# Kernel optimization log

Measured on AMD Instinct MI355X. Metric: run time of the kernel, lower is better.

Reference implementation:

```python
import jax, jax.numpy as jnp
import numpy as np

B, T, D, H = 128, 512, 64, 512  # batch, seq_len, feature dim, hidden dim
S_MIN, S_FRAC = 0.5, 0.5        # aug_args for generate_samp_mask


def setup_inputs() -> dict:
    key = jax.random.key(0)
    ks = jax.random.split(key, 8)
    x = jax.random.normal(ks[0], (B, T, D), jnp.float32)
    # monotonically increasing irregular timestamps
    tp = jnp.cumsum(jax.random.uniform(ks[1], (B, T), jnp.float32, 1e-3, 0.1), axis=1)
    # Deterministic replay of generate_samp_mask: mask[i]=1 -> teacher forcing
    rng = np.random.default_rng(0)
    extrap_ind = int(rng.integers(int(T * S_MIN), T))
    samp_inds = np.sort(rng.choice(np.arange(extrap_ind), int(S_FRAC * extrap_ind), replace=False))
    mask = np.zeros(T, dtype=np.int32)
    mask[samp_inds] = 1
    samp_mask = jnp.asarray(mask)
    s = 1.0 / np.sqrt(H)  # torch GRUCell/Linear default uniform init scale
    W_ih = jax.random.uniform(ks[2], (3 * H, D + 1), jnp.float32, -s, s)
    W_hh = jax.random.uniform(ks[3], (3 * H, H), jnp.float32, -s, s)
    b_ih = jax.random.uniform(ks[4], (3 * H,), jnp.float32, -s, s)
    b_hh = jax.random.uniform(ks[5], (3 * H,), jnp.float32, -s, s)
    W_out = jax.random.uniform(ks[6], (H, D), jnp.float32, -s, s)
    b_out = jax.random.uniform(ks[7], (D,), jnp.float32, -s, s)
    return {"x": x, "tp": tp, "samp_mask": samp_mask, "W_ih": W_ih, "W_hh": W_hh,
            "b_ih": b_ih, "b_hh": b_hh, "W_out": W_out, "b_out": b_out}


def _gru_cell(inp, h, W_ih, W_hh, b_ih, b_hh):
    gi = inp @ W_ih.T + b_ih          # (B, 3H)
    gh = h @ W_hh.T + b_hh            # (B, 3H)
    i_r, i_z, i_n = jnp.split(gi, 3, axis=-1)
    h_r, h_z, h_n = jnp.split(gh, 3, axis=-1)
    r = jax.nn.sigmoid(i_r + h_r)
    z = jax.nn.sigmoid(i_z + h_z)
    n = jnp.tanh(i_n + r * h_n)
    return (1.0 - z) * n + z * h


def reference(x, tp, samp_mask, W_ih, W_hh, b_ih, b_hh, W_out, b_out):
    # delta_t: append time deltas as an extra channel
    offset = jnp.concatenate([jnp.zeros((tp.shape[0], 1), tp.dtype), tp[:, :-1]], axis=1)
    delta = (tp - offset)[..., None]            # (B, T, 1)
    xin = jnp.concatenate([x, delta], axis=-1)  # (B, T, D+1)

    def step(h, inputs):
        x_t, m = inputs                          # (B, D+1), scalar bool
        prev_out = h @ W_out + b_out             # (B, D)
        ar_in = jnp.concatenate([prev_out, x_t[:, -2:-1]], axis=-1)  # (B, D+1)
        inp = jnp.where(m, x_t, ar_in)
        h_new = _gru_cell(inp, h, W_ih, W_hh, b_ih, b_hh)
        return h_new, h_new

    h0 = jnp.zeros((x.shape[0], H), x.dtype)
    _, h_arr = jax.lax.scan(step, h0, (jnp.swapaxes(xin, 0, 1), samp_mask.astype(bool)))
    h_arr = jnp.swapaxes(h_arr, 0, 1)            # (B, T, H)
    out = h_arr @ W_out + b_out                  # (B, T, D)
    # select_by_length with lens == T for every sample -> flat (B*T, D)
    return out.reshape(-1, out.shape[-1])
```

## Files before the change

kernel.cpp:

```cpp
#include <hip/hip_runtime.h>
#include <math.h>

#define TB 512

typedef __attribute__((ext_vector_type(8))) short bf16x8;
typedef __attribute__((ext_vector_type(4))) float f32x4;
typedef unsigned long long u64;

#define BW_B   0
#define AH_B   98304
#define PRE_F  32768
#define XPRE_F 33824
#define ORED_F 34616
#define WOC_F  35160
#define WIH_F  35672
#define SB_F   37256
#define XLAST_F 37352
#define MSK_F  37384
#define LDS_FLOATS 37896
#define LDS_BYTES (LDS_FLOATS * 4)

#define STEP_BYTES 262144
#define GRP_BYTES  65536
#define HIST_NEEDED (4096ull + 513ull * STEP_BYTES)
#define PLANE_STRIDE 262144
#define FB_NEEDED (4096ull + 2ull * PLANE_STRIDE)

__device__ __forceinline__ unsigned rne16(float f) {
  unsigned u = __float_as_uint(f);
  return (u + 0x7FFFu + ((u >> 16) & 1u)) >> 16;
}
__device__ __forceinline__ float bfhilo(unsigned hh, unsigned hl) {
  return __uint_as_float(hh << 16) + __uint_as_float(hl << 16);
}

__global__ __launch_bounds__(TB) void gru_persistent(
    const float* __restrict__ x, const float* __restrict__ tp, const int* __restrict__ mask,
    const float* __restrict__ W_ih, const float* __restrict__ W_hh,
    const float* __restrict__ b_ih, const float* __restrict__ b_hh,
    const float* __restrict__ W_out, const float* __restrict__ b_out,
    char* __restrict__ data, unsigned* __restrict__ ctr,
    float* __restrict__ out, int hmode)
{
  extern __shared__ char smem[];
  float* LP = (float*)smem;
  int* MSK = (int*)&LP[MSK_F];
  const int tid = threadIdx.x;
  const int wg  = blockIdx.x;
  const int s   = wg & 63;
  const int g   = wg >> 6;
  const int bg0 = g * 32;
  const int j0  = 8 * s;
  const int lane = tid & 63;
  const int wv   = tid >> 6;

  unsigned short* planes = (unsigned short*)data;

  MSK[tid] = mask[tid];
  if (tid < 65) {
    for (int p = 0; p < 24; ++p) {
      int row = (p < 8) ? (j0 + p) : (p < 16) ? (512 + j0 + (p - 8)) : (1024 + j0 + (p - 16));
      LP[WIH_F + p * 66 + tid] = W_ih[(size_t)row * 65 + tid];
    }
  }
  LP[WOC_F + tid] = W_out[(size_t)tid * 64 + s];
  if (tid < 16) {
    int row = (tid < 8) ? (j0 + tid) : (512 + j0 + (tid - 8));
    const float* wi = W_ih + (size_t)row * 65;
    float bt = b_ih[row] + b_hh[row];
    float bp = 0.f;
    for (int d = 0; d < 64; ++d) bp = fmaf(wi[d], b_out[d], bp);
    LP[SB_F + tid]      = bt;
    LP[SB_F + 16 + tid] = bt + bp;
    LP[SB_F + 32 + tid] = wi[64];
  } else if (tid < 24) {
    int jj = tid - 16;
    int row = 1024 + j0 + jj;
    const float* wi = W_ih + (size_t)row * 65;
    float bp = 0.f;
    for (int d = 0; d < 64; ++d) bp = fmaf(wi[d], b_out[d], bp);
    LP[SB_F + 48 + jj] = b_hh[row];
    LP[SB_F + 56 + jj] = b_ih[row];
    LP[SB_F + 64 + jj] = b_ih[row] + bp;
    LP[SB_F + 72 + jj] = wi[64];
  }
  if (tid == 0) LP[SB_F + 80] = b_out[s];

  if (tid < 32) {
    if (hmode) {
      const int half = tid >> 4, ln = (tid & 15) | ((s & 3) << 4), ks = s >> 2;
      char* dst = data + (size_t)g * GRP_BYTES;
      u64* c0 = (u64*)(dst + (size_t)(((0 * 16 + ks) * 2 + half) * 64 + ln) * 16);
      u64* c1 = (u64*)(dst + (size_t)(((1 * 16 + ks) * 2 + half) * 64 + ln) * 16);
      __hip_atomic_store(c0,     0ull, __ATOMIC_RELAXED, __HIP_MEMORY_SCOPE_AGENT);
      __hip_atomic_store(c0 + 1, 0ull, __ATOMIC_RELAXED, __HIP_MEMORY_SCOPE_AGENT);
      __hip_atomic_store(c1,     0ull, __ATOMIC_RELAXED, __HIP_MEMORY_SCOPE_AGENT);
      __hip_atomic_store(c1 + 1, 0ull, __ATOMIC_RELAXED, __HIP_MEMORY_SCOPE_AGENT);
    } else {
      u64* hh0 = (u64*)(planes + (size_t)(bg0 + tid) * 512 + j0);
      u64* hl0 = (u64*)(planes + 65536 + (size_t)(bg0 + tid) * 512 + j0);
      __hip_atomic_store(hh0,     0ull, __ATOMIC_RELAXED, __HIP_MEMORY_SCOPE_AGENT);
      __hip_atomic_store(hh0 + 1, 0ull, __ATOMIC_RELAXED, __HIP_MEMORY_SCOPE_AGENT);
      __hip_atomic_store(hl0,     0ull, __ATOMIC_RELAXED, __HIP_MEMORY_SCOPE_AGENT);
      __hip_atomic_store(hl0 + 1, 0ull, __ATOMIC_RELAXED, __HIP_MEMORY_SCOPE_AGENT);
    }
  }
  __syncthreads();

  {
    const int k = tid;
    const float* wo = W_out + (size_t)k * 64;
    unsigned short* bw16 = (unsigned short*)(smem + BW_B);
    for (int rr = 0; rr < 48; ++rr) {
      int c, col; float w;
      if (rr < 16) {
        c = 1; col = rr;
        int row = (rr < 8) ? (j0 + rr) : (512 + j0 + rr - 8);
        w = W_hh[(size_t)row * 512 + k];
      } else if (rr < 24) {
        c = 0; col = rr - 16;
        w = W_hh[(size_t)(1024 + j0 + rr - 16) * 512 + k];
      } else {
        int p, whrow;
        if (rr < 32) { c = 0; col = rr - 24 + 8; p = 16 + (rr - 24); whrow = -1; }
        else if (rr < 40) { c = 2; col = rr - 32; p = rr - 32; whrow = j0 + rr - 32; }
        else { c = 2; col = rr - 40 + 8; p = 8 + (rr - 40); whrow = 512 + j0 + rr - 40; }
        const float* wr = &LP[WIH_F + p * 66];
        float a = 0.f;
#pragma unroll 8
        for (int d = 0; d < 64; ++d) a = fmaf(wr[d], wo[d], a);
        w = a + (whrow >= 0 ? W_hh[(size_t)whrow * 512 + k] : 0.f);
      }
      unsigned wh = rne16(w);
      float resid = w - __uint_as_float(wh << 16);
      unsigned wl = rne16(resid);
      int base = c * 32768 + (k >> 5) * 1024 + (col | (((k >> 3) & 3) << 4)) * 16 + (k & 7) * 2;
      bw16[base >> 1] = (unsigned short)wh;
      bw16[(base + 16384) >> 1] = (unsigned short)wl;
    }
  }
  __syncthreads();

  auto stage_x = [&](int tt) {
    if (tt >= 512) return;
    if (MSK[tt] != 0) {
      for (int task = tid; task < 768; task += TB) {
        const int xr = task >> 5, b = task & 31;
        const float* wrow = &LP[WIH_F + xr * 66];
        size_t ti = (size_t)(bg0 + b) * 512 + tt;
        float del = tp[ti] - (tt > 0 ? tp[ti - 1] : 0.f);
        float xa = wrow[64] * del;
        const float4* x4 = (const float4*)(x + ti * 64);
#pragma unroll
        for (int d4 = 0; d4 < 16; ++d4) {
          float4 xv = x4[d4];
          xa = fmaf(wrow[d4 * 4 + 0], xv.x, xa);
          xa = fmaf(wrow[d4 * 4 + 1], xv.y, xa);
          xa = fmaf(wrow[d4 * 4 + 2], xv.z, xa);
          xa = fmaf(wrow[d4 * 4 + 3], xv.w, xa);
        }
        LP[XPRE_F + xr * 33 + b] = xa;
      }
    } else if (tid < 32) {
      LP[XLAST_F + tid] = x[((size_t)(bg0 + tid) * 512 + tt) * 64 + 63];
    }
  };

  stage_x(0);

  unsigned target = 64;
  unsigned* myctr = &ctr[g * 64];

  asm volatile("s_waitcnt vmcnt(0)" ::: "memory");
  __syncthreads();
  if (tid == 0) {
    __hip_atomic_fetch_add(myctr, 1u, __ATOMIC_RELAXED, __HIP_MEMORY_SCOPE_AGENT);
    int cnt = 0;
    while (__hip_atomic_load(myctr, __ATOMIC_RELAXED, __HIP_MEMORY_SCOPE_AGENT) < target) {
      __builtin_amdgcn_s_sleep(2);
      if (++cnt > 16384) break;
    }
  }
  __syncthreads();
  target += 64;

  const unsigned short* ah16 = (const unsigned short*)(smem + AH_B);

  for (int t = 0; t <= 512; ++t) {
    const bool last = (t == 512);
    const bool teacher = (!last) && (MSK[t] != 0);
    const int csel = teacher ? 1 : 2;

    uint4 h0v[4], h1v[4];
    if (hmode) {
      const char* src = data + (size_t)t * STEP_BYTES + (size_t)g * GRP_BYTES;
#pragma unroll
      for (int i = 0; i < 4; ++i) {
        int c = i * 512 + tid;
        int sg = c >> 6, ln = c & 63;
        h0v[i] = *(const uint4*)(src + (size_t)((sg * 2 + 0) * 64 + ln) * 16);
        h1v[i] = *(const uint4*)(src + (size_t)((sg * 2 + 1) * 64 + ln) * 16);
      }
    } else {
      const int cur = t & 1;
      const unsigned short* HHc = planes + (size_t)cur * (PLANE_STRIDE / 2);
      const unsigned short* HLc = HHc + 65536;
#pragma unroll
      for (int i = 0; i < 4; ++i) {
        int c = i * 512 + tid;
        int sg = c >> 6, ln = c & 63;
        int term = sg >> 4, ks = sg & 15;
        const unsigned short* pl = term ? HLc : HHc;
        const unsigned short* src0 = pl + ((size_t)(bg0 + (ln & 15)) * 512 + ks * 32 + ((ln >> 4) & 3) * 8);
        const u64* p0 = (const u64*)src0;
        const u64* p1 = (const u64*)(src0 + 16 * 512);
        u64 a0 = __hip_atomic_load(p0,     __ATOMIC_RELAXED, __HIP_MEMORY_SCOPE_AGENT);
        u64 a1 = __hip_atomic_load(p0 + 1, __ATOMIC_RELAXED, __HIP_MEMORY_SCOPE_AGENT);
        u64 b0 = __hip_atomic_load(p1,     __ATOMIC_RELAXED, __HIP_MEMORY_SCOPE_AGENT);
        u64 b1 = __hip_atomic_load(p1 + 1, __ATOMIC_RELAXED, __HIP_MEMORY_SCOPE_AGENT);
        h0v[i] = uint4{(unsigned)a0, (unsigned)(a0 >> 32), (unsigned)a1, (unsigned)(a1 >> 32)};
        h1v[i] = uint4{(unsigned)b0, (unsigned)(b0 >> 32), (unsigned)b1, (unsigned)(b1 >> 32)};
      }
    }
#pragma unroll
    for (int i = 0; i < 4; ++i) {
      int c = i * 512 + tid;
      *(uint4*)(smem + AH_B + (size_t)c * 16) = h0v[i];
    }
    __syncthreads();

    float hp = 0.f;
    for (int half = 0; half < 2; ++half) {
      const int rtoff = half * 16;

      if (!last && wv < 2) {
        const int cslot = (wv == 0) ? 0 : csel;
        const char* bb = smem + BW_B + cslot * 32768;
        const char* ab = smem + AH_B;
        f32x4 acc0 = {0.f, 0.f, 0.f, 0.f};
        f32x4 acc1 = {0.f, 0.f, 0.f, 0.f};
        f32x4 acc2 = {0.f, 0.f, 0.f, 0.f};
        f32x4 acc3 = {0.f, 0.f, 0.f, 0.f};
#pragma unroll
        for (int ks4 = 0; ks4 < 4; ++ks4) {
#pragma unroll
          for (int q4 = 0; q4 < 4; ++q4) {
            int ks = ks4 * 4 + q4;
            bf16x8 ahh = *(const bf16x8*)(ab + ks * 1024 + lane * 16);
            bf16x8 ahl = *(const bf16x8*)(ab + (16 + ks) * 1024 + lane * 16);
            bf16x8 bhh = *(const bf16x8*)(bb + ks * 1024 + lane * 16);
            bf16x8 bhl = *(const bf16x8*)(bb + (16 + ks) * 1024 + lane * 16);
            f32x4& acc = (q4 == 0) ? acc0 : (q4 == 1) ? acc1 : (q4 == 2) ? acc2 : acc3;
            acc = __builtin_amdgcn_mfma_f32_16x16x32_bf16(ahh, bhh, acc, 0, 0, 0);
            acc = __builtin_amdgcn_mfma_f32_16x16x32_bf16(ahh, bhl, acc, 0, 0, 0);
            acc = __builtin_amdgcn_mfma_f32_16x16x32_bf16(ahl, bhh, acc, 0, 0, 0);
          }
        }
        f32x4 accA = acc0 + acc1;
        f32x4 accB = acc2 + acc3;
        f32x4 acc = accA + accB;
        const int prow = ((wv == 0) ? 16 : 0) + (lane & 15);
        const int pcol = rtoff + ((lane >> 4) << 2);
#pragma unroll
        for (int q = 0; q < 4; ++q) LP[PRE_F + prow * 33 + pcol + q] = acc[q];
      }

      if (tid >= 128 && tid < 384) {
        const int tA = tid - 128;
        const int bl = tA & 15, ks = tA >> 4;
        const int b = rtoff + bl;
        const float* woc = &LP[WOC_F];
        float oa = 0.f;
#pragma unroll
        for (int c = 0; c < 4; ++c) {
          const uint4 wh = *(const uint4*)(smem + AH_B + ks * 1024 + (bl | (c << 4)) * 16);
          const uint4 wl = *(const uint4*)(smem + AH_B + (16 + ks) * 1024 + (bl | (c << 4)) * 16);
          int k0 = ks * 32 + c * 8;
          oa = fmaf(bfhilo(wh.x & 0xFFFFu, wl.x & 0xFFFFu), woc[k0 + 0], oa);
          oa = fmaf(bfhilo(wh.x >> 16, wl.x >> 16), woc[k0 + 1], oa);
          oa = fmaf(bfhilo(wh.y & 0xFFFFu, wl.y & 0xFFFFu), woc[k0 + 2], oa);
          oa = fmaf(bfhilo(wh.y >> 16, wl.y >> 16), woc[k0 + 3], oa);
          oa = fmaf(bfhilo(wh.z & 0xFFFFu, wl.z & 0xFFFFu), woc[k0 + 4], oa);
          oa = fmaf(bfhilo(wh.z >> 16, wl.z >> 16), woc[k0 + 5], oa);
          oa = fmaf(bfhilo(wh.w & 0xFFFFu, wl.w & 0xFFFFu), woc[k0 + 6], oa);
          oa = fmaf(bfhilo(wh.w >> 16, wl.w >> 16), woc[k0 + 7], oa);
        }
        LP[ORED_F + b * 17 + ks] = oa;
      }

      if (tid < 256 && (((tid & 31) >> 4) == half)) {
        const int b = tid & 31, jj = tid >> 5;
        const int k = j0 + jj;
        const int ks = k >> 5, e = k & 7;
        const int ln = (b & 15) | (((k >> 3) & 3) << 4);
        unsigned hh = ah16[(ks * 1024 + ln * 16 + e * 2) >> 1];
        unsigned hl = ah16[((16 + ks) * 1024 + ln * 16 + e * 2) >> 1];
        hp = bfhilo(hh, hl);
      }
      __syncthreads();
      if (half == 0) {
#pragma unroll
        for (int i = 0; i < 4; ++i) {
          int c = i * 512 + tid;
          *(uint4*)(smem + AH_B + (size_t)c * 16) = h1v[i];
        }
        __syncthreads();
      }
    }

    if (!last && tid < 256) {
      const int b = tid & 31, jj = tid >> 5;
      float pr = LP[PRE_F + jj * 33 + b];
      float pz = LP[PRE_F + (8 + jj) * 33 + b];
      float pnh = LP[PRE_F + (16 + jj) * 33 + b] + LP[SB_F + 48 + jj];
      float pni;
      if (teacher) {
        pr += LP[XPRE_F + jj * 33 + b] + LP[SB_F + jj];
        pz += LP[XPRE_F + (8 + jj) * 33 + b] + LP[SB_F + 8 + jj];
        pni = LP[XPRE_F + (16 + jj) * 33 + b] + LP[SB_F + 56 + jj];
      } else {
        float xl = LP[XLAST_F + b];
        pr += LP[SB_F + 16 + jj] + LP[SB_F + 32 + jj] * xl;
        pz += LP[SB_F + 24 + jj] + LP[SB_F + 40 + jj] * xl;
        pni = LP[PRE_F + (24 + jj) * 33 + b] + LP[SB_F + 64 + jj] + LP[SB_F + 72 + jj] * xl;
      }
      float rg = 1.f / (1.f + expf(-pr));
      float zg = 1.f / (1.f + expf(-pz));
      float ng = tanhf(fmaf(rg, pnh, pni));
      float hv = fmaf(zg, hp - ng, ng);
      float hvp = __shfl_xor(hv, 32, 64);
      if ((jj & 1) == 0) {
        unsigned h0h = rne16(hv), h1h = rne16(hvp);
        float r0 = hv  - __uint_as_float(h0h << 16);
        float r1 = hvp - __uint_as_float(h1h << 16);
        unsigned hw = h0h | (h1h << 16);
        unsigned lw = rne16(r0) | (rne16(r1) << 16);
        unsigned *dhh, *dhl;
        if (hmode) {
          char* dst = data + (size_t)(t + 1) * STEP_BYTES + (size_t)g * GRP_BYTES;
          const int half = b >> 4, ln = (b & 15) | ((s & 3) << 4), ks = s >> 2;
          dhh = (unsigned*)(dst + (size_t)(((0 * 16 + ks) * 2 + half) * 64 + ln) * 16 + jj * 2);
          dhl = (unsigned*)(dst + (size_t)(((1 * 16 + ks) * 2 + half) * 64 + ln) * 16 + jj * 2);
        } else {
          const int cur = t & 1;
          unsigned short* HHn = (unsigned short*)(planes + (size_t)(cur ^ 1) * (PLANE_STRIDE / 2));
          unsigned short* HLn = HHn + 65536;
          dhh = (unsigned*)(HHn + (size_t)(bg0 + b) * 512 + j0 + jj);
          dhl = (unsigned*)(HLn + (size_t)(bg0 + b) * 512 + j0 + jj);
        }
        __hip_atomic_store(dhh, hw, __ATOMIC_RELAXED, __HIP_MEMORY_SCOPE_AGENT);
        __hip_atomic_store(dhl, lw, __ATOMIC_RELAXED, __HIP_MEMORY_SCOPE_AGENT);
      }
    }

    if (!last) {
      asm volatile("s_waitcnt vmcnt(0)" ::: "memory");
      __syncthreads();
      if (tid == 0)
        __hip_atomic_fetch_add(myctr, 1u, __ATOMIC_RELAXED, __HIP_MEMORY_SCOPE_AGENT);
      if (t >= 1 && tid >= 256 && tid < 288) {
        const int b = tid - 256;
        float o = LP[SB_F + 80];
#pragma unroll
        for (int i = 0; i < 16; ++i) o += LP[ORED_F + b * 17 + i];
        out[((size_t)(bg0 + b) * 512 + (t - 1)) * 64 + s] = o;
      }
      stage_x(t + 1);
      if (tid == 0) {
        int cnt = 0;
        while (__hip_atomic_load(myctr, __ATOMIC_RELAXED, __HIP_MEMORY_SCOPE_AGENT) < target) {
          __builtin_amdgcn_s_sleep(2);
          if (++cnt > 16384) break;
        }
      }
      __syncthreads();
      target += 64;
    } else {
      if (tid >= 256 && tid < 288) {
        const int b = tid - 256;
        float o = LP[SB_F + 80];
#pragma unroll
        for (int i = 0; i < 16; ++i) o += LP[ORED_F + b * 17 + i];
        out[((size_t)(bg0 + b) * 512 + 511) * 64 + s] = o;
      }
    }
  }
}

extern "C" void kernel_launch(void* const* d_in, const int* in_sizes, int n_in,
                              void* d_out, int out_size, void* d_ws, size_t ws_size,
                              hipStream_t stream) {
  (void)in_sizes; (void)n_in; (void)out_size;
  const float* x    = (const float*)d_in[0];
  const float* tp   = (const float*)d_in[1];
  const int*   mask = (const int*)d_in[2];
  const float* W_ih = (const float*)d_in[3];
  const float* W_hh = (const float*)d_in[4];
  const float* b_ih = (const float*)d_in[5];
  const float* b_hh = (const float*)d_in[6];
  const float* W_out= (const float*)d_in[7];
  const float* b_out= (const float*)d_in[8];
  float* out = (float*)d_out;
  if (ws_size < FB_NEEDED) return;
  int hmode = (ws_size >= HIST_NEEDED) ? 1 : 0;
  unsigned* ctr = (unsigned*)d_ws;
  char* dataptr = (char*)d_ws + 4096;
  hipMemsetAsync(ctr, 0, 4096, stream);
  hipFuncSetAttribute((const void*)gru_persistent,
                      hipFuncAttributeMaxDynamicSharedMemorySize, LDS_BYTES);
  hipLaunchKernelGGL(gru_persistent, dim3(256), dim3(TB), LDS_BYTES, stream,
                     x, tp, mask, W_ih, W_hh, b_ih, b_hh, W_out, b_out, dataptr, ctr, out, hmode);
}
```

Before: 3.473 ms.

## Keep GRU weights in registers, split MFMA over six waves, use per-block flags

Each of six waves now loads its slice of the recurrent weight matrix (hi/lo bf16) into registers once, before the time loop. The K dimension is split between wave pairs, with partial sums reduced in LDS, so both batch halves are processed in a single pass with fewer barriers. The shared atomic counter barrier is replaced by per-block monotonic flags that one wave polls with a ballot. The fallback buffer uses the same tiled layout as the history mode. This aims to cut per-step LDS weight traffic, barrier count and counter contention, at the cost of higher register pressure (launch bounds now request 2 blocks) and more polling loads.

```diff
diff --git a/kernel.cpp b/kernel.cpp
--- a/kernel.cpp
+++ b/kernel.cpp
@@ -7,24 +7,22 @@
 typedef __attribute__((ext_vector_type(4))) float f32x4;
 typedef unsigned long long u64;
 
-#define BW_B   0
-#define AH_B   98304
-#define PRE_F  32768
-#define XPRE_F 33824
-#define ORED_F 34616
-#define WOC_F  35160
-#define WIH_F  35672
-#define SB_F   37256
-#define XLAST_F 37352
-#define MSK_F  37384
-#define LDS_FLOATS 37896
+#define FBASE  24576
+#define PREP_F (FBASE)
+#define XPRE_F (FBASE + 2112)
+#define ORED_F (FBASE + 2904)
+#define WOC_F  (FBASE + 3448)
+#define WIH_F  (FBASE + 3960)
+#define SB_F   (FBASE + 5544)
+#define XLAST_F (FBASE + 5640)
+#define MSK_F  (FBASE + 5672)
+#define LDS_FLOATS (FBASE + 6184)
 #define LDS_BYTES (LDS_FLOATS * 4)
 
 #define STEP_BYTES 262144
 #define GRP_BYTES  65536
 #define HIST_NEEDED (4096ull + 513ull * STEP_BYTES)
-#define PLANE_STRIDE 262144
-#define FB_NEEDED (4096ull + 2ull * PLANE_STRIDE)
+#define FB_NEEDED   (4096ull + 2ull * STEP_BYTES)
 
 __device__ __forceinline__ unsigned rne16(float f) {
   unsigned u = __float_as_uint(f);
@@ -34,12 +32,12 @@
   return __uint_as_float(hh << 16) + __uint_as_float(hl << 16);
 }
 
-__global__ __launch_bounds__(TB) void gru_persistent(
+__global__ __launch_bounds__(TB, 2) void gru_persistent(
     const float* __restrict__ x, const float* __restrict__ tp, const int* __restrict__ mask,
     const float* __restrict__ W_ih, const float* __restrict__ W_hh,
     const float* __restrict__ b_ih, const float* __restrict__ b_hh,
     const float* __restrict__ W_out, const float* __restrict__ b_out,
-    char* __restrict__ data, unsigned* __restrict__ ctr,
+    char* __restrict__ data, unsigned* __restrict__ flags,
     float* __restrict__ out, int hmode)
 {
   extern __shared__ char smem[];
@@ -53,8 +51,7 @@
   const int j0  = 8 * s;
   const int lane = tid & 63;
   const int wv   = tid >> 6;
-
-  unsigned short* planes = (unsigned short*)data;
+  const int myct = wv >> 1, mykh = wv & 1;
 
   MSK[tid] = mask[tid];
   if (tid < 65) {
@@ -85,32 +82,17 @@
     LP[SB_F + 72 + jj] = wi[64];
   }
   if (tid == 0) LP[SB_F + 80] = b_out[s];
-
-  if (tid < 32) {
-    if (hmode) {
-      const int half = tid >> 4, ln = (tid & 15) | ((s & 3) << 4), ks = s >> 2;
-      char* dst = data + (size_t)g * GRP_BYTES;
-      u64* c0 = (u64*)(dst + (size_t)(((0 * 16 + ks) * 2 + half) * 64 + ln) * 16);
-      u64* c1 = (u64*)(dst + (size_t)(((1 * 16 + ks) * 2 + half) * 64 + ln) * 16);
-      __hip_atomic_store(c0,     0ull, __ATOMIC_RELAXED, __HIP_MEMORY_SCOPE_AGENT);
-      __hip_atomic_store(c0 + 1, 0ull, __ATOMIC_RELAXED, __HIP_MEMORY_SCOPE_AGENT);
-      __hip_atomic_store(c1,     0ull, __ATOMIC_RELAXED, __HIP_MEMORY_SCOPE_AGENT);
-      __hip_atomic_store(c1 + 1, 0ull, __ATOMIC_RELAXED, __HIP_MEMORY_SCOPE_AGENT);
-    } else {
-      u64* hh0 = (u64*)(planes + (size_t)(bg0 + tid) * 512 + j0);
-      u64* hl0 = (u64*)(planes + 65536 + (size_t)(bg0 + tid) * 512 + j0);
-      __hip_atomic_store(hh0,     0ull, __ATOMIC_RELAXED, __HIP_MEMORY_SCOPE_AGENT);
-      __hip_atomic_store(hh0 + 1, 0ull, __ATOMIC_RELAXED, __HIP_MEMORY_SCOPE_AGENT);
-      __hip_atomic_store(hl0,     0ull, __ATOMIC_RELAXED, __HIP_MEMORY_SCOPE_AGENT);
-      __hip_atomic_store(hl0 + 1, 0ull, __ATOMIC_RELAXED, __HIP_MEMORY_SCOPE_AGENT);
-    }
+  if (tid < 64) {
+    u64* p = (u64*)(data + (size_t)g * GRP_BYTES + (size_t)s * 1024 + tid * 16);
+    __hip_atomic_store(p,     0ull, __ATOMIC_RELAXED, __HIP_MEMORY_SCOPE_AGENT);
+    __hip_atomic_store(p + 1, 0ull, __ATOMIC_RELAXED, __HIP_MEMORY_SCOPE_AGENT);
   }
   __syncthreads();
 
   {
     const int k = tid;
     const float* wo = W_out + (size_t)k * 64;
-    unsigned short* bw16 = (unsigned short*)(smem + BW_B);
+    unsigned short* bw16 = (unsigned short*)smem;
     for (int rr = 0; rr < 48; ++rr) {
       int c, col; float w;
       if (rr < 16) {
@@ -141,6 +123,15 @@
   }
   __syncthreads();
 
+  bf16x8 Bh[8], Bl[8];
+  if (wv < 6) {
+#pragma unroll
+    for (int i = 0; i < 8; ++i) {
+      Bh[i] = *(const bf16x8*)(smem + myct * 32768 + (mykh * 8 + i) * 1024 + lane * 16);
+      Bl[i] = *(const bf16x8*)(smem + myct * 32768 + 16384 + (mykh * 8 + i) * 1024 + lane * 16);
+    }
+  }
+
   auto stage_x = [&](int tt) {
     if (tt >= 512) return;
     if (MSK[tt] != 0) {
@@ -168,113 +159,110 @@
 
   stage_x(0);
 
-  unsigned target = 64;
-  unsigned* myctr = &ctr[g * 64];
+  unsigned* myflags = &flags[g * 64];
 
   asm volatile("s_waitcnt vmcnt(0)" ::: "memory");
   __syncthreads();
-  if (tid == 0) {
-    __hip_atomic_fetch_add(myctr, 1u, __ATOMIC_RELAXED, __HIP_MEMORY_SCOPE_AGENT);
+  if (tid == 0)
+    __hip_atomic_store(&myflags[s], 1u, __ATOMIC_RELAXED, __HIP_MEMORY_SCOPE_AGENT);
+  if (wv == 0) {
     int cnt = 0;
-    while (__hip_atomic_load(myctr, __ATOMIC_RELAXED, __HIP_MEMORY_SCOPE_AGENT) < target) {
-      __builtin_amdgcn_s_sleep(2);
-      if (++cnt > 16384) break;
+    while (true) {
+      unsigned v = __hip_atomic_load(&myflags[lane], __ATOMIC_RELAXED, __HIP_MEMORY_SCOPE_AGENT);
+      if (__ballot(v < 1u) == 0ull) break;
+      __builtin_amdgcn_s_sleep(1);
+      if (++cnt > 500000) break;
     }
   }
   __syncthreads();
-  target += 64;
-
-  const unsigned short* ah16 = (const unsigned short*)(smem + AH_B);
+
+  const unsigned short* ah16 = (const unsigned short*)smem;
 
   for (int t = 0; t <= 512; ++t) {
     const bool last = (t == 512);
     const bool teacher = (!last) && (MSK[t] != 0);
     const int csel = teacher ? 1 : 2;
 
-    uint4 h0v[4], h1v[4];
+    const char* src = data + (size_t)(hmode ? t : (t & 1)) * STEP_BYTES + (size_t)g * GRP_BYTES;
+    uint4 v0[4], v1[4];
     if (hmode) {
-      const char* src = data + (size_t)t * STEP_BYTES + (size_t)g * GRP_BYTES;
 #pragma unroll
       for (int i = 0; i < 4; ++i) {
-        int c = i * 512 + tid;
-        int sg = c >> 6, ln = c & 63;
-        h0v[i] = *(const uint4*)(src + (size_t)((sg * 2 + 0) * 64 + ln) * 16);
-        h1v[i] = *(const uint4*)(src + (size_t)((sg * 2 + 1) * 64 + ln) * 16);
+        int c = i * 512 + tid, sg = c >> 6, ln = c & 63;
+        v0[i] = *(const uint4*)(src + (size_t)((sg * 2 + 0) * 64 + ln) * 16);
+        v1[i] = *(const uint4*)(src + (size_t)((sg * 2 + 1) * 64 + ln) * 16);
       }
     } else {
-      const int cur = t & 1;
-      const unsigned short* HHc = planes + (size_t)cur * (PLANE_STRIDE / 2);
-      const unsigned short* HLc = HHc + 65536;
 #pragma unroll
       for (int i = 0; i < 4; ++i) {
-        int c = i * 512 + tid;
-        int sg = c >> 6, ln = c & 63;
-        int term = sg >> 4, ks = sg & 15;
-        const unsigned short* pl = term ? HLc : HHc;
-        const unsigned short* src0 = pl + ((size_t)(bg0 + (ln & 15)) * 512 + ks * 32 + ((ln >> 4) & 3) * 8);
-        const u64* p0 = (const u64*)src0;
-        const u64* p1 = (const u64*)(src0 + 16 * 512);
+        int c = i * 512 + tid, sg = c >> 6, ln = c & 63;
+        const u64* p0 = (const u64*)(src + (size_t)((sg * 2 + 0) * 64 + ln) * 16);
+        const u64* p1 = (const u64*)(src + (size_t)((sg * 2 + 1) * 64 + ln) * 16);
         u64 a0 = __hip_atomic_load(p0,     __ATOMIC_RELAXED, __HIP_MEMORY_SCOPE_AGENT);
         u64 a1 = __hip_atomic_load(p0 + 1, __ATOMIC_RELAXED, __HIP_MEMORY_SCOPE_AGENT);
         u64 b0 = __hip_atomic_load(p1,     __ATOMIC_RELAXED, __HIP_MEMORY_SCOPE_AGENT);
         u64 b1 = __hip_atomic_load(p1 + 1, __ATOMIC_RELAXED, __HIP_MEMORY_SCOPE_AGENT);
-        h0v[i] = uint4{(unsigned)a0, (unsigned)(a0 >> 32), (unsigned)a1, (unsigned)(a1 >> 32)};
-        h1v[i] = uint4{(unsigned)b0, (unsigned)(b0 >> 32), (unsigned)b1, (unsigned)(b1 >> 32)};
+        v0[i] = uint4{(unsigned)a0, (unsigned)(a0 >> 32), (unsigned)a1, (unsigned)(a1 >> 32)};
+        v1[i] = uint4{(unsigned)b0, (unsigned)(b0 >> 32), (unsigned)b1, (unsigned)(b1 >> 32)};
       }
     }
 #pragma unroll
     for (int i = 0; i < 4; ++i) {
-      int c = i * 512 + tid;
-      *(uint4*)(smem + AH_B + (size_t)c * 16) = h0v[i];
+      int c = i * 512 + tid, sg = c >> 6, ln = c & 63;
+      *(uint4*)(smem + (size_t)(sg * 1024) + ln * 16)        = v0[i];
+      *(uint4*)(smem + (size_t)((32 + sg) * 1024) + ln * 16) = v1[i];
     }
     __syncthreads();
 
     float hp = 0.f;
-    for (int half = 0; half < 2; ++half) {
-      const int rtoff = half * 16;
-
-      if (!last && wv < 2) {
-        const int cslot = (wv == 0) ? 0 : csel;
-        const char* bb = smem + BW_B + cslot * 32768;
-        const char* ab = smem + AH_B;
+    if (tid < 256) {
+      const int b = tid & 31, jj = tid >> 5;
+      const int ks = s >> 2, half = b >> 4;
+      const int ln = (b & 15) | ((s & 3) << 4);
+      unsigned hh = ah16[((half * 32 + ks) * 1024 + ln * 16 + jj * 2) >> 1];
+      unsigned hl = ah16[((half * 32 + 16 + ks) * 1024 + ln * 16 + jj * 2) >> 1];
+      hp = bfhilo(hh, hl);
+    }
+
+    if (!last && wv < 6 && (myct == 0 || myct == csel)) {
+#pragma unroll
+      for (int half = 0; half < 2; ++half) {
         f32x4 acc0 = {0.f, 0.f, 0.f, 0.f};
         f32x4 acc1 = {0.f, 0.f, 0.f, 0.f};
         f32x4 acc2 = {0.f, 0.f, 0.f, 0.f};
         f32x4 acc3 = {0.f, 0.f, 0.f, 0.f};
 #pragma unroll
-        for (int ks4 = 0; ks4 < 4; ++ks4) {
-#pragma unroll
-          for (int q4 = 0; q4 < 4; ++q4) {
-            int ks = ks4 * 4 + q4;
-            bf16x8 ahh = *(const bf16x8*)(ab + ks * 1024 + lane * 16);
-            bf16x8 ahl = *(const bf16x8*)(ab + (16 + ks) * 1024 + lane * 16);
-            bf16x8 bhh = *(const bf16x8*)(bb + ks * 1024 + lane * 16);
-            bf16x8 bhl = *(const bf16x8*)(bb + (16 + ks) * 1024 + lane * 16);
-            f32x4& acc = (q4 == 0) ? acc0 : (q4 == 1) ? acc1 : (q4 == 2) ? acc2 : acc3;
-            acc = __builtin_amdgcn_mfma_f32_16x16x32_bf16(ahh, bhh, acc, 0, 0, 0);
-            acc = __builtin_amdgcn_mfma_f32_16x16x32_bf16(ahh, bhl, acc, 0, 0, 0);
-            acc = __builtin_amdgcn_mfma_f32_16x16x32_bf16(ahl, bhh, acc, 0, 0, 0);
-          }
-        }
-        f32x4 accA = acc0 + acc1;
-        f32x4 accB = acc2 + acc3;
-        f32x4 acc = accA + accB;
-        const int prow = ((wv == 0) ? 16 : 0) + (lane & 15);
-        const int pcol = rtoff + ((lane >> 4) << 2);
-#pragma unroll
-        for (int q = 0; q < 4; ++q) LP[PRE_F + prow * 33 + pcol + q] = acc[q];
-      }
-
-      if (tid >= 128 && tid < 384) {
-        const int tA = tid - 128;
-        const int bl = tA & 15, ks = tA >> 4;
-        const int b = rtoff + bl;
+        for (int i = 0; i < 8; ++i) {
+          const char* abh = smem + (size_t)((half * 32 + mykh * 8 + i) * 1024) + lane * 16;
+          bf16x8 ahh = *(const bf16x8*)abh;
+          bf16x8 ahl = *(const bf16x8*)(abh + 16 * 1024);
+          f32x4& acc = ((i & 3) == 0) ? acc0 : ((i & 3) == 1) ? acc1 : ((i & 3) == 2) ? acc2 : acc3;
+          acc = __builtin_amdgcn_mfma_f32_16x16x32_bf16(ahh, Bh[i], acc, 0, 0, 0);
+          acc = __builtin_amdgcn_mfma_f32_16x16x32_bf16(ahh, Bl[i], acc, 0, 0, 0);
+          acc = __builtin_amdgcn_mfma_f32_16x16x32_bf16(ahl, Bh[i], acc, 0, 0, 0);
+        }
+        f32x4 acc = (acc0 + acc1) + (acc2 + acc3);
+        const int prow = (myct == 0 ? 16 : 0) + (lane & 15);
+        const int pcol = half * 16 + ((lane >> 4) << 2);
+#pragma unroll
+        for (int q = 0; q < 4; ++q)
+          LP[PREP_F + mykh * 1056 + prow * 33 + pcol + q] = acc[q];
+      }
+    }
+
+    if (wv >= 6) {
+#pragma unroll
+      for (int tk = 0; tk < 4; ++tk) {
+        const int task = (tid - 384) + tk * 128;
+        const int half = task >> 8, rem = task & 255;
+        const int bl = rem & 15, ks = rem >> 4;
+        const int b = half * 16 + bl;
         const float* woc = &LP[WOC_F];
         float oa = 0.f;
 #pragma unroll
         for (int c = 0; c < 4; ++c) {
-          const uint4 wh = *(const uint4*)(smem + AH_B + ks * 1024 + (bl | (c << 4)) * 16);
-          const uint4 wl = *(const uint4*)(smem + AH_B + (16 + ks) * 1024 + (bl | (c << 4)) * 16);
+          const uint4 wh = *(const uint4*)(smem + (size_t)((half * 32 + ks) * 1024) + (bl | (c << 4)) * 16);
+          const uint4 wl = *(const uint4*)(smem + (size_t)((half * 32 + 16 + ks) * 1024) + (bl | (c << 4)) * 16);
           int k0 = ks * 32 + c * 8;
           oa = fmaf(bfhilo(wh.x & 0xFFFFu, wl.x & 0xFFFFu), woc[k0 + 0], oa);
           oa = fmaf(bfhilo(wh.x >> 16, wl.x >> 16), woc[k0 + 1], oa);
@@ -287,77 +275,53 @@
         }
         LP[ORED_F + b * 17 + ks] = oa;
       }
-
-      if (tid < 256 && (((tid & 31) >> 4) == half)) {
+    }
+    __syncthreads();
+
+    if (!last) {
+      if (tid < 256) {
         const int b = tid & 31, jj = tid >> 5;
-        const int k = j0 + jj;
-        const int ks = k >> 5, e = k & 7;
-        const int ln = (b & 15) | (((k >> 3) & 3) << 4);
-        unsigned hh = ah16[(ks * 1024 + ln * 16 + e * 2) >> 1];
-        unsigned hl = ah16[((16 + ks) * 1024 + ln * 16 + e * 2) >> 1];
-        hp = bfhilo(hh, hl);
-      }
-      __syncthreads();
-      if (half == 0) {
-#pragma unroll
-        for (int i = 0; i < 4; ++i) {
-          int c = i * 512 + tid;
-          *(uint4*)(smem + AH_B + (size_t)c * 16) = h1v[i];
-        }
-        __syncthreads();
-      }
-    }
-
-    if (!last && tid < 256) {
-      const int b = tid & 31, jj = tid >> 5;
-      float pr = LP[PRE_F + jj * 33 + b];
-      float pz = LP[PRE_F + (8 + jj) * 33 + b];
-      float pnh = LP[PRE_F + (16 + jj) * 33 + b] + LP[SB_F + 48 + jj];
-      float pni;
-      if (teacher) {
-        pr += LP[XPRE_F + jj * 33 + b] + LP[SB_F + jj];
-        pz += LP[XPRE_F + (8 + jj) * 33 + b] + LP[SB_F + 8 + jj];
-        pni = LP[XPRE_F + (16 + jj) * 33 + b] + LP[SB_F + 56 + jj];
-      } else {
-        float xl = LP[XLAST_F + b];
-        pr += LP[SB_F + 16 + jj] + LP[SB_F + 32 + jj] * xl;
-        pz += LP[SB_F + 24 + jj] + LP[SB_F + 40 + jj] * xl;
-        pni = LP[PRE_F + (24 + jj) * 33 + b] + LP[SB_F + 64 + jj] + LP[SB_F + 72 + jj] * xl;
-      }
-      float rg = 1.f / (1.f + expf(-pr));
-      float zg = 1.f / (1.f + expf(-pz));
-      float ng = tanhf(fmaf(rg, pnh, pni));
-      float hv = fmaf(zg, hp - ng, ng);
-      float hvp = __shfl_xor(hv, 32, 64);
-      if ((jj & 1) == 0) {
-        unsigned h0h = rne16(hv), h1h = rne16(hvp);
-        float r0 = hv  - __uint_as_float(h0h << 16);
-        float r1 = hvp - __uint_as_float(h1h << 16);
-        unsigned hw = h0h | (h1h << 16);
-        unsigned lw = rne16(r0) | (rne16(r1) << 16);
-        unsigned *dhh, *dhl;
-        if (hmode) {
-          char* dst = data + (size_t)(t + 1) * STEP_BYTES + (size_t)g * GRP_BYTES;
-          const int half = b >> 4, ln = (b & 15) | ((s & 3) << 4), ks = s >> 2;
-          dhh = (unsigned*)(dst + (size_t)(((0 * 16 + ks) * 2 + half) * 64 + ln) * 16 + jj * 2);
-          dhl = (unsigned*)(dst + (size_t)(((1 * 16 + ks) * 2 + half) * 64 + ln) * 16 + jj * 2);
+        float pr  = LP[PREP_F + jj * 33 + b]        + LP[PREP_F + 1056 + jj * 33 + b];
+        float pz  = LP[PREP_F + (8 + jj) * 33 + b]  + LP[PREP_F + 1056 + (8 + jj) * 33 + b];
+        float pnh = LP[PREP_F + (16 + jj) * 33 + b] + LP[PREP_F + 1056 + (16 + jj) * 33 + b]
+                  + LP[SB_F + 48 + jj];
+        float pni;
+        if (teacher) {
+          pr += LP[XPRE_F + jj * 33 + b] + LP[SB_F + jj];
+          pz += LP[XPRE_F + (8 + jj) * 33 + b] + LP[SB_F + 8 + jj];
+          pni = LP[XPRE_F + (16 + jj) * 33 + b] + LP[SB_F + 56 + jj];
         } else {
-          const int cur = t & 1;
-          unsigned short* HHn = (unsigned short*)(planes + (size_t)(cur ^ 1) * (PLANE_STRIDE / 2));
-          unsigned short* HLn = HHn + 65536;
-          dhh = (unsigned*)(HHn + (size_t)(bg0 + b) * 512 + j0 + jj);
-          dhl = (unsigned*)(HLn + (size_t)(bg0 + b) * 512 + j0 + jj);
-        }
-        __hip_atomic_store(dhh, hw, __ATOMIC_RELAXED, __HIP_MEMORY_SCOPE_AGENT);
-        __hip_atomic_store(dhl, lw, __ATOMIC_RELAXED, __HIP_MEMORY_SCOPE_AGENT);
-      }
-    }
-
-    if (!last) {
+          float xl = LP[XLAST_F + b];
+          pr += LP[SB_F + 16 + jj] + LP[SB_F + 32 + jj] * xl;
+          pz += LP[SB_F + 24 + jj] + LP[SB_F + 40 + jj] * xl;
+          pni = LP[PREP_F + (24 + jj) * 33 + b] + LP[PREP_F + 1056 + (24 + jj) * 33 + b]
+              + LP[SB_F + 64 + jj] + LP[SB_F + 72 + jj] * xl;
+        }
+        float rg = 1.f / (1.f + expf(-pr));
+        float zg = 1.f / (1.f + expf(-pz));
+        float ng = tanhf(fmaf(rg, pnh, pni));
+        float hv = fmaf(zg, hp - ng, ng);
+        float hvp = __shfl_xor(hv, 32, 64);
+        if ((jj & 1) == 0) {
+          unsigned h0h = rne16(hv), h1h = rne16(hvp);
+          float r0 = hv  - __uint_as_float(h0h << 16);
+          float r1 = hvp - __uint_as_float(h1h << 16);
+          unsigned hw = h0h | (h1h << 16);
+          unsigned lw = rne16(r0) | (rne16(r1) << 16);
+          char* dst = data + (size_t)(hmode ? (t + 1) : ((t + 1) & 1)) * STEP_BYTES
+                    + (size_t)g * GRP_BYTES;
+          const int half = b >> 4, ln2 = (b & 15) | ((s & 3) << 4), ks2 = s >> 2;
+          unsigned* dhh = (unsigned*)(dst + (size_t)((ks2 * 2 + half) * 64 + ln2) * 16 + jj * 2);
+          unsigned* dhl = (unsigned*)(dst + (size_t)(((16 + ks2) * 2 + half) * 64 + ln2) * 16 + jj * 2);
+          __hip_atomic_store(dhh, hw, __ATOMIC_RELAXED, __HIP_MEMORY_SCOPE_AGENT);
+          __hip_atomic_store(dhl, lw, __ATOMIC_RELAXED, __HIP_MEMORY_SCOPE_AGENT);
+        }
+      }
       asm volatile("s_waitcnt vmcnt(0)" ::: "memory");
       __syncthreads();
+      const unsigned tgt = (unsigned)(t + 2);
       if (tid == 0)
-        __hip_atomic_fetch_add(myctr, 1u, __ATOMIC_RELAXED, __HIP_MEMORY_SCOPE_AGENT);
+        __hip_atomic_store(&myflags[s], tgt, __ATOMIC_RELAXED, __HIP_MEMORY_SCOPE_AGENT);
       if (t >= 1 && tid >= 256 && tid < 288) {
         const int b = tid - 256;
         float o = LP[SB_F + 80];
@@ -366,15 +330,16 @@
         out[((size_t)(bg0 + b) * 512 + (t - 1)) * 64 + s] = o;
       }
       stage_x(t + 1);
-      if (tid == 0) {
+      if (wv == 0) {
         int cnt = 0;
-        while (__hip_atomic_load(myctr, __ATOMIC_RELAXED, __HIP_MEMORY_SCOPE_AGENT) < target) {
-          __builtin_amdgcn_s_sleep(2);
-          if (++cnt > 16384) break;
+        while (true) {
+          unsigned v = __hip_atomic_load(&myflags[lane], __ATOMIC_RELAXED, __HIP_MEMORY_SCOPE_AGENT);
+          if (__ballot(v < tgt) == 0ull) break;
+          __builtin_amdgcn_s_sleep(1);
+          if (++cnt > 200000) break;
         }
       }
       __syncthreads();
-      target += 64;
     } else {
       if (tid >= 256 && tid < 288) {
         const int b = tid - 256;
@@ -403,11 +368,11 @@
   float* out = (float*)d_out;
   if (ws_size < FB_NEEDED) return;
   int hmode = (ws_size >= HIST_NEEDED) ? 1 : 0;
-  unsigned* ctr = (unsigned*)d_ws;
+  unsigned* flags = (unsigned*)d_ws;
   char* dataptr = (char*)d_ws + 4096;
-  hipMemsetAsync(ctr, 0, 4096, stream);
+  hipMemsetAsync(flags, 0, 4096, stream);
   hipFuncSetAttribute((const void*)gru_persistent,
                       hipFuncAttributeMaxDynamicSharedMemorySize, LDS_BYTES);
   hipLaunchKernelGGL(gru_persistent, dim3(256), dim3(TB), LDS_BYTES, stream,
-                     x, tp, mask, W_ih, W_hh, b_ih, b_hh, W_out, b_out, dataptr, ctr, out, hmode);
+                     x, tp, mask, W_ih, W_hh, b_ih, b_hh, W_out, b_out, dataptr, flags, out, hmode);
 }
```

New measurement: 3.396 ms. 2.2% less time.
